# Performance work log

Measured on AMD Instinct MI355X. Metric: run time of the kernel, lower is better.

The kernel has to match this reference:

```python
import jax, jax.numpy as jnp
import numpy as np

HIDDEN = 1024
N_HEADS = 16
HEAD_DIM = HIDDEN // N_HEADS


def setup_inputs() -> dict:
    key = jax.random.key(0)
    ks = jax.random.split(key, 7)
    b, l, m = 4, 1024, 1024
    q = jax.random.normal(ks[0], (b, l, HIDDEN), dtype=jnp.float32)
    k = jax.random.normal(ks[1], (b, m, HIDDEN), dtype=jnp.float32)
    v = jax.random.normal(ks[2], (b, m, HIDDEN), dtype=jnp.float32)
    s = 1.0 / np.sqrt(HIDDEN)
    w_q = jax.random.normal(ks[3], (HIDDEN, HIDDEN), dtype=jnp.float32) * s
    w_k = jax.random.normal(ks[4], (HIDDEN, HIDDEN), dtype=jnp.float32) * s
    w_v = jax.random.normal(ks[5], (HIDDEN, HIDDEN), dtype=jnp.float32) * s
    w_o = jax.random.normal(ks[6], (HIDDEN, HIDDEN), dtype=jnp.float32) * s
    return {"q": q, "k": k, "v": v, "w_q": w_q, "w_k": w_k, "w_v": w_v, "w_o": w_o}


def reference(q, k, v, w_q, w_k, w_v, w_o):
    b, l, _ = q.shape
    _, m, _ = k.shape
    # Linear (bias=False): y = x @ W^T
    qp = q @ w_q.T
    kp = k @ w_k.T
    vp = v @ w_v.T  # projected but unused downstream (faithful to original bug)
    # Faithful non-standard split: hidden -> (head_dim, n_heads)
    qh = qp.reshape(b, l, HEAD_DIM, N_HEADS)
    kh = kp.reshape(b, m, HEAD_DIM, N_HEADS)
    # attn over K, scaled, softmax over m (dim=2)
    scores = jnp.einsum('bldn,bmdn->blmn', qh, kh) / np.sqrt(HEAD_DIM)
    attn = jax.nn.softmax(scores, axis=2)
    # dropout is identity in eval mode
    # NOTE: original attends over K (not V) — reproduced faithfully
    x = jnp.einsum('blmn,bmdn->bldn', attn, kh)
    x = x.reshape(b, l, HIDDEN)  # 'b l d n -> b l (d n)'
    return x @ w_o.T
```

## Files before the change

kernel.cpp:

```cpp
#include <hip/hip_runtime.h>
#include <hip/hip_bf16.h>
#include <stdint.h>
#include <math.h>


typedef __bf16 bf16;
typedef __bf16 bf16x8 __attribute__((ext_vector_type(8)));
typedef float  f32x4  __attribute__((ext_vector_type(4)));

__device__ __forceinline__ void async_load16(const void* g, void* l) {
  __builtin_amdgcn_global_load_lds((__attribute__((address_space(1))) void*)g,
                                   (__attribute__((address_space(3))) void*)l,
                                   16, 0, 0);
}

__device__ __forceinline__ int detect_fl(const void* samp, int tid, int* smax) {
  int e = (((const unsigned short*)samp)[tid] >> 7) & 0xFF;
#pragma unroll
  for (int off = 1; off <= 32; off <<= 1) {
    int o = __shfl_xor(e, off);
    e = o > e ? o : e;
  }
  if ((tid & 63) == 0) smax[tid >> 6] = e;
  __syncthreads();
  int m01 = smax[0] > smax[1] ? smax[0] : smax[1];
  int m23 = smax[2] > smax[3] ? smax[2] : smax[3];
  return ((m01 > m23 ? m01 : m23) >= 140) ? 1 : 0;
}

__global__ void __launch_bounds__(256)
canon_wo(const void* __restrict__ wo_raw, bf16* __restrict__ wo_p,
         int* __restrict__ flag) {
  __shared__ int smax[4];
  const int tid = threadIdx.x;
  const int fl = detect_fl(wo_raw, tid, smax);
  if (blockIdx.x == 0 && tid == 0) *flag = fl;

  int d0 = blockIdx.x * 2048 + tid * 8;
  int o = d0 >> 10, kp0 = d0 & 1023;
  bf16x8 v;
#pragma unroll
  for (int j = 0; j < 8; ++j) {
    int kp = kp0 + j;
    int h = ((kp & 63) << 4) | (kp >> 6);
    float f = fl ? ((const float*)wo_raw)[o * 1024 + h]
                 : (float)((const bf16*)wo_raw)[o * 1024 + h];
    f = fminf(fmaxf(f, -1024.f), 1024.f);
    v[j] = (bf16)f;
  }
  *(bf16x8*)(wo_p + d0) = v;
}

__global__ void __launch_bounds__(256, 2)
qk_gemm(const void* __restrict__ q_raw, const void* __restrict__ wq_raw,
        const void* __restrict__ k_raw, const void* __restrict__ wk_raw,
        bf16* __restrict__ qh, bf16* __restrict__ kh, bf16* __restrict__ khT,
        float cs) {
  __shared__ bf16 sA[128 * 64];
  __shared__ bf16 sB[128 * 64];
  __shared__ bf16 epi[128 * 134];
  __shared__ int smax[4];

  const int tid = threadIdx.x;
  const int fl  = detect_fl(q_raw, tid, smax);

  const int z = blockIdx.z;
  const void* A = z ? k_raw : q_raw;
  const void* W = z ? wk_raw : wq_raw;
  const float scale = z ? 1.0f : cs;
  bf16* out0 = z ? kh : qh;

  const int lane = tid & 63;
  const int wave = tid >> 6;
  const int q4   = lane >> 4;
  const int c16  = lane & 15;
  const int wm   = wave >> 1;
  const int wn   = wave & 1;

  const int lin    = blockIdx.x + 8 * blockIdx.y;
  const int rowBlk = (lin & 31) * 128;
  const int colBlk = (lin >> 5) * 128;

  int sr[4], sg[4];
#pragma unroll
  for (int i = 0; i < 4; ++i) {
    int s = tid + 256 * i;
    sr[i] = s >> 3;
    sg[i] = (s & 7) ^ (sr[i] & 7);
  }

  f32x4 acc[4][4] = {};

  for (int kk = 0; kk < 1024; kk += 64) {
    __syncthreads();
    {
      bf16x8 st[4];
      if (fl) {
#pragma unroll
        for (int i = 0; i < 4; ++i) {
          const float* p = (const float*)A +
              (size_t)(rowBlk + sr[i]) * 1024 + kk + sg[i] * 8;
#pragma unroll
          for (int j = 0; j < 8; ++j) st[i][j] = (bf16)p[j];
        }
      } else {
#pragma unroll
        for (int i = 0; i < 4; ++i)
          st[i] = *(const bf16x8*)((const bf16*)A +
              (size_t)(rowBlk + sr[i]) * 1024 + kk + sg[i] * 8);
      }
#pragma unroll
      for (int i = 0; i < 4; ++i) *(bf16x8*)(sA + (tid + 256 * i) * 8) = st[i];
    }
    {
      bf16x8 st[4];
      if (fl) {
#pragma unroll
        for (int i = 0; i < 4; ++i) {
          const float* p = (const float*)W +
              (size_t)(colBlk + sr[i]) * 1024 + kk + sg[i] * 8;
#pragma unroll
          for (int j = 0; j < 8; ++j) st[i][j] = (bf16)p[j];
        }
      } else {
#pragma unroll
        for (int i = 0; i < 4; ++i)
          st[i] = *(const bf16x8*)((const bf16*)W +
              (size_t)(colBlk + sr[i]) * 1024 + kk + sg[i] * 8);
      }
#pragma unroll
      for (int i = 0; i < 4; ++i) *(bf16x8*)(sB + (tid + 256 * i) * 8) = st[i];
    }
    __syncthreads();

    bf16x8 af[2][4], bfr[2][4];
#pragma unroll
    for (int ks = 0; ks < 2; ++ks) {
#pragma unroll
      for (int mt = 0; mt < 4; ++mt) {
        int row = wm * 64 + mt * 16 + c16;
        af[ks][mt] = *(const bf16x8*)(sA + row * 64 +
                       (((ks * 4 + q4) ^ (row & 7)) * 8));
      }
#pragma unroll
      for (int nt = 0; nt < 4; ++nt) {
        int row = wn * 64 + nt * 16 + c16;
        bfr[ks][nt] = *(const bf16x8*)(sB + row * 64 +
                       (((ks * 4 + q4) ^ (row & 7)) * 8));
      }
    }
#pragma unroll
    for (int ks = 0; ks < 2; ++ks)
#pragma unroll
      for (int mt = 0; mt < 4; ++mt)
#pragma unroll
        for (int nt = 0; nt < 4; ++nt)
          acc[mt][nt] = __builtin_amdgcn_mfma_f32_16x16x32_bf16(
              af[ks][mt], bfr[ks][nt], acc[mt][nt], 0, 0, 0);
  }

  __syncthreads();
#pragma unroll
  for (int mt = 0; mt < 4; ++mt)
#pragma unroll
    for (int nt = 0; nt < 4; ++nt)
#pragma unroll
      for (int r = 0; r < 4; ++r) {
        int m_t = wm * 64 + mt * 16 + q4 * 4 + r;
        int h_t = wn * 64 + nt * 16 + c16;
        epi[m_t * 134 + h_t] = (bf16)(acc[mt][nt][r] * scale);
      }
  __syncthreads();

  const int bb    = rowBlk >> 10;
  const int mbase = rowBlk & 1023;
  const int dg0   = colBlk >> 4;

  {
    int n = tid >> 4;
#pragma unroll
    for (int i = 0; i < 8; ++i) {
      int m_t = (tid & 15) + i * 16;
      bf16x8 v;
#pragma unroll
      for (int dt = 0; dt < 8; ++dt) v[dt] = epi[m_t * 134 + dt * 16 + n];
      *(bf16x8*)(out0 + ((size_t)(bb * 16 + n) * 1024 + mbase + m_t) * 64 + dg0) = v;
    }
  }
  if (z) {
    int h_t = tid >> 1, half = tid & 1;
    int n = h_t & 15, dt = h_t >> 4;
    size_t base = ((size_t)(bb * 16 + n) * 64 + dg0 + dt) * 1024 + mbase + half * 64;
#pragma unroll
    for (int c = 0; c < 8; ++c) {
      bf16x8 v;
#pragma unroll
      for (int j = 0; j < 8; ++j) v[j] = epi[(half * 64 + c * 8 + j) * 134 + h_t];
      *(bf16x8*)(khT + base + c * 8) = v;
    }
  }
}

__global__ void __launch_bounds__(256, 2)
o_gemm(const bf16* __restrict__ A, const bf16* __restrict__ W,
       bf16* __restrict__ out0, float* __restrict__ outf,
       const int* __restrict__ flag) {
  __shared__ bf16 sA[128 * 128];
  __shared__ bf16 sB[64 * 128];

  const int tid  = threadIdx.x;
  const int lane = tid & 63;
  const int wave = tid >> 6;
  const int q4   = lane >> 4;
  const int c16  = lane & 15;
  const int wm   = wave >> 1;
  const int wn   = wave & 1;

  const int lin    = blockIdx.x + 16 * blockIdx.y;
  const int rowBlk = (lin & 31) * 128;
  const int colBlk = (lin >> 5) * 64;

  int ar[8], ag[8];
#pragma unroll
  for (int i = 0; i < 8; ++i) {
    int s = tid + 256 * i;
    ar[i] = s >> 4;
    ag[i] = (s & 15) ^ (ar[i] & 15);
  }
  const bf16* gA[8];
  bf16* lA[8];
#pragma unroll
  for (int i = 0; i < 8; ++i) {
    gA[i] = A + (size_t)(rowBlk + ar[i]) * 1024 + ag[i] * 8;
    lA[i] = sA + (tid + 256 * i) * 8;
  }
  const bf16* gB[4];
  bf16* lB[4];
#pragma unroll
  for (int i = 0; i < 4; ++i) {
    int s = tid + 256 * i;
    int br = s >> 4, bg = (s & 15) ^ (br & 15);
    gB[i] = W + (size_t)(colBlk + br) * 1024 + bg * 8;
    lB[i] = sB + s * 8;
  }

  f32x4 acc[4][2] = {};

  for (int kk = 0; kk < 1024; kk += 128) {
    __syncthreads();
#pragma unroll
    for (int i = 0; i < 8; ++i) async_load16(gA[i] + kk, lA[i]);
#pragma unroll
    for (int i = 0; i < 4; ++i) async_load16(gB[i] + kk, lB[i]);
    __builtin_amdgcn_s_waitcnt(0);
    __syncthreads();

#pragma unroll
    for (int ks = 0; ks < 4; ++ks) {
      bf16x8 af[4], bfr[2];
#pragma unroll
      for (int mt = 0; mt < 4; ++mt) {
        int row = wm * 64 + mt * 16 + c16;
        af[mt] = *(const bf16x8*)(sA + row * 128 +
                   (((ks * 4 + q4) ^ (row & 15)) * 8));
      }
#pragma unroll
      for (int nt = 0; nt < 2; ++nt) {
        int row = wn * 32 + nt * 16 + c16;
        bfr[nt] = *(const bf16x8*)(sB + row * 128 +
                   (((ks * 4 + q4) ^ (row & 15)) * 8));
      }
#pragma unroll
      for (int mt = 0; mt < 4; ++mt)
#pragma unroll
        for (int nt = 0; nt < 2; ++nt)
          acc[mt][nt] = __builtin_amdgcn_mfma_f32_16x16x32_bf16(
              af[mt], bfr[nt], acc[mt][nt], 0, 0, 0);
    }
  }

  const int fl = *flag;
#pragma unroll
  for (int mt = 0; mt < 4; ++mt)
#pragma unroll
    for (int nt = 0; nt < 2; ++nt)
#pragma unroll
      for (int r = 0; r < 4; ++r) {
        int gm = rowBlk + wm * 64 + mt * 16 + q4 * 4 + r;
        int gn = colBlk + wn * 32 + nt * 16 + c16;
        size_t idx = (size_t)gm * 1024 + gn;
        if (fl) outf[idx] = acc[mt][nt][r];
        else    out0[idx] = (bf16)acc[mt][nt][r];
      }
}

__global__ void __launch_bounds__(256, 2)
attn_kernel(const bf16* __restrict__ qh, const bf16* __restrict__ kh,
            const bf16* __restrict__ khT, bf16* __restrict__ xh) {
  __shared__ bf16 sK[128 * 64];
  __shared__ bf16 sKT[64 * 128];
  __shared__ bf16 sP[4][32 * 136];

  const int tid  = threadIdx.x;
  const int lane = tid & 63;
  const int wave = tid >> 6;
  const int q4   = lane >> 4;
  const int c16  = lane & 15;
  const int bn   = blockIdx.x;
  const int b    = bn >> 4, n = bn & 15;
  const int l0w  = blockIdx.y * 128 + wave * 32;

  const bf16* qhead  = qh  + (size_t)bn * (1024 * 64);
  const bf16* khead  = kh  + (size_t)bn * (1024 * 64);
  const bf16* kThead = khT + (size_t)bn * (64 * 1024);

  bf16x8 aq[2][2];
#pragma unroll
  for (int g = 0; g < 2; ++g)
#pragma unroll
    for (int hh = 0; hh < 2; ++hh)
      aq[g][hh] = *(const bf16x8*)(qhead +
                    (size_t)(l0w + g * 16 + c16) * 64 + hh * 32 + q4 * 8);

  int kr[4], kg[4], tr[4], tg[4];
#pragma unroll
  for (int i = 0; i < 4; ++i) {
    int s = tid + 256 * i;
    kr[i] = s >> 3;  kg[i] = (s & 7) ^ (kr[i] & 7);
    tr[i] = s >> 4;  tg[i] = (s & 15) ^ (tr[i] & 15);
  }

  f32x4 O[2][4] = {};
  f32x4 Osum[2] = {};
  bf16x8 ones;
#pragma unroll
  for (int j = 0; j < 8; ++j) ones[j] = (bf16)1.0f;
  bf16* sPw = sP[wave];

  for (int m0 = 0; m0 < 1024; m0 += 128) {
    __syncthreads();
#pragma unroll
    for (int i = 0; i < 4; ++i) {
      async_load16(khead + (size_t)(m0 + kr[i]) * 64 + kg[i] * 8,
                   sK + (tid + 256 * i) * 8);
      async_load16(kThead + (size_t)tr[i] * 1024 + m0 + tg[i] * 8,
                   sKT + (tid + 256 * i) * 8);
    }
    __builtin_amdgcn_s_waitcnt(0);
    __syncthreads();

    f32x4 S[2][8] = {};
#pragma unroll
    for (int t = 0; t < 8; ++t) {
#pragma unroll
      for (int hh = 0; hh < 2; ++hh) {
        int row = t * 16 + c16;
        bf16x8 bk = *(const bf16x8*)(sK + row * 64 +
                                     (((hh * 4 + q4) ^ (row & 7)) * 8));
        S[0][t] = __builtin_amdgcn_mfma_f32_16x16x32_bf16(aq[0][hh], bk, S[0][t], 0, 0, 0);
        S[1][t] = __builtin_amdgcn_mfma_f32_16x16x32_bf16(aq[1][hh], bk, S[1][t], 0, 0, 0);
      }
    }

#pragma unroll
    for (int g = 0; g < 2; ++g)
#pragma unroll
      for (int t = 0; t < 8; ++t)
#pragma unroll
        for (int r = 0; r < 4; ++r) {
          float p = __builtin_amdgcn_exp2f(S[g][t][r]);
          sPw[(g * 16 + q4 * 4 + r) * 136 + t * 16 + c16] = (bf16)p;
        }

    bf16x8 ap[2][4];
#pragma unroll
    for (int g = 0; g < 2; ++g) {
#pragma unroll
      for (int kk2 = 0; kk2 < 4; ++kk2) {
        ap[g][kk2] = *(const bf16x8*)(sPw + (g * 16 + c16) * 136 +
                                      kk2 * 32 + q4 * 8);
        Osum[g] = __builtin_amdgcn_mfma_f32_16x16x32_bf16(ap[g][kk2], ones, Osum[g], 0, 0, 0);
      }
    }

#pragma unroll
    for (int td = 0; td < 4; ++td) {
#pragma unroll
      for (int kk2 = 0; kk2 < 4; ++kk2) {
        int row = td * 16 + c16;
        bf16x8 bkt = *(const bf16x8*)(sKT + row * 128 +
                                      (((kk2 * 4 + q4) ^ (row & 15)) * 8));
        O[0][td] = __builtin_amdgcn_mfma_f32_16x16x32_bf16(ap[0][kk2], bkt, O[0][td], 0, 0, 0);
        O[1][td] = __builtin_amdgcn_mfma_f32_16x16x32_bf16(ap[1][kk2], bkt, O[1][td], 0, 0, 0);
      }
    }
  }

#pragma unroll
  for (int g = 0; g < 2; ++g) {
    float inv[4];
#pragma unroll
    for (int r = 0; r < 4; ++r) inv[r] = 1.0f / Osum[g][r];
#pragma unroll
    for (int td = 0; td < 4; ++td)
#pragma unroll
      for (int r = 0; r < 4; ++r)
        sPw[(g * 16 + q4 * 4 + r) * 136 + td * 16 + c16] = (bf16)(O[g][td][r] * inv[r]);
  }
  {
    int l_loc = lane >> 2, dq = lane & 3;
#pragma unroll
    for (int g = 0; g < 2; ++g) {
      bf16x8 v0 = *(const bf16x8*)(sPw + (g * 16 + l_loc) * 136 + dq * 16);
      bf16x8 v1 = *(const bf16x8*)(sPw + (g * 16 + l_loc) * 136 + dq * 16 + 8);
      size_t base = ((size_t)(b * 1024 + l0w + g * 16 + l_loc) * 16 + n) * 64 + dq * 16;
      *(bf16x8*)(xh + base)     = v0;
      *(bf16x8*)(xh + base + 8) = v1;
    }
  }
}

extern "C" void kernel_launch(void* const* d_in, const int* in_sizes, int n_in,
                              void* d_out, int out_size, void* d_ws, size_t ws_size,
                              hipStream_t stream) {
  const void* q_raw  = d_in[0];
  const void* k_raw  = d_in[1];
  const void* wq_raw = d_in[3];
  const void* wk_raw = d_in[4];
  const void* wo_raw = d_in[6];

  char* ws = (char*)d_ws;
  const size_t MB = 1024 * 1024;
  bf16* xh   = (bf16*)(ws + 0 * MB);
  bf16* kh   = (bf16*)(ws + 16 * MB);
  bf16* wo_p = (bf16*)(ws + 28 * MB);
  int*  flag = (int*)(ws + 30 * MB);
  bf16* qh   = (bf16*)d_out;
  bf16* khT  = (bf16*)((char*)d_out + 8 * MB);

  const float CS = 0.125f * 1.4426950408889634f;
  dim3 blk(256, 1, 1);

  hipLaunchKernelGGL(canon_wo, dim3(512), blk, 0, stream,
                     wo_raw, wo_p, flag);
  hipLaunchKernelGGL(qk_gemm, dim3(8, 32, 2), blk, 0, stream,
                     q_raw, wq_raw, k_raw, wk_raw, qh, kh, khT, CS);
  hipLaunchKernelGGL(attn_kernel, dim3(64, 8, 1), blk, 0, stream,
                     qh, kh, khT, xh);
  hipLaunchKernelGGL(o_gemm, dim3(16, 32, 1), blk, 0, stream,
                     xh, wo_p, (bf16*)d_out, (float*)d_out, flag);
}
```

Measured before the change: 188.7 us.

## Prefetch next fp32 K-tile into registers and use async LDS loads for bf16 path

The projection GEMM's main loop is split by input type. In the fp32 path, the next 64-wide K slice of A and W is loaded into registers with vectorized f32x4 loads while the current tile's MFMAs run, so global latency overlaps with compute; conversion to bf16 happens just before the LDS store. In the bf16 path, global_load_lds async copies replace the register round trip. The register prefetch raises VGPR pressure and may reduce occupancy, and the bf16 path still waits fully before computing.

```diff
diff --git a/kernel.cpp b/kernel.cpp
--- a/kernel.cpp
+++ b/kernel.cpp
@@ -91,72 +91,112 @@
 
   f32x4 acc[4][4] = {};
 
-  for (int kk = 0; kk < 1024; kk += 64) {
-    __syncthreads();
-    {
-      bf16x8 st[4];
-      if (fl) {
+  if (fl) {
+    const float* Af = (const float*)A;
+    const float* Wf = (const float*)W;
+    f32x4 stA[8], stB[8];
+#pragma unroll
+    for (int i = 0; i < 4; ++i) {
+      const float* pA = Af + (size_t)(rowBlk + sr[i]) * 1024 + sg[i] * 8;
+      stA[2 * i]     = *(const f32x4*)pA;
+      stA[2 * i + 1] = *(const f32x4*)(pA + 4);
+      const float* pB = Wf + (size_t)(colBlk + sr[i]) * 1024 + sg[i] * 8;
+      stB[2 * i]     = *(const f32x4*)pB;
+      stB[2 * i + 1] = *(const f32x4*)(pB + 4);
+    }
+
+    for (int kk = 0; kk < 1024; kk += 64) {
+      __syncthreads();
+#pragma unroll
+      for (int i = 0; i < 4; ++i) {
+        bf16x8 va, vb;
+#pragma unroll
+        for (int j = 0; j < 4; ++j) {
+          va[j]     = (bf16)stA[2 * i][j];
+          va[4 + j] = (bf16)stA[2 * i + 1][j];
+          vb[j]     = (bf16)stB[2 * i][j];
+          vb[4 + j] = (bf16)stB[2 * i + 1][j];
+        }
+        *(bf16x8*)(sA + (tid + 256 * i) * 8) = va;
+        *(bf16x8*)(sB + (tid + 256 * i) * 8) = vb;
+      }
+      __syncthreads();
+
+      if (kk + 64 < 1024) {
 #pragma unroll
         for (int i = 0; i < 4; ++i) {
-          const float* p = (const float*)A +
-              (size_t)(rowBlk + sr[i]) * 1024 + kk + sg[i] * 8;
-#pragma unroll
-          for (int j = 0; j < 8; ++j) st[i][j] = (bf16)p[j];
-        }
-      } else {
-#pragma unroll
-        for (int i = 0; i < 4; ++i)
-          st[i] = *(const bf16x8*)((const bf16*)A +
-              (size_t)(rowBlk + sr[i]) * 1024 + kk + sg[i] * 8);
-      }
-#pragma unroll
-      for (int i = 0; i < 4; ++i) *(bf16x8*)(sA + (tid + 256 * i) * 8) = st[i];
-    }
-    {
-      bf16x8 st[4];
-      if (fl) {
-#pragma unroll
-        for (int i = 0; i < 4; ++i) {
-          const float* p = (const float*)W +
-              (size_t)(colBlk + sr[i]) * 1024 + kk + sg[i] * 8;
-#pragma unroll
-          for (int j = 0; j < 8; ++j) st[i][j] = (bf16)p[j];
-        }
-      } else {
-#pragma unroll
-        for (int i = 0; i < 4; ++i)
-          st[i] = *(const bf16x8*)((const bf16*)W +
-              (size_t)(colBlk + sr[i]) * 1024 + kk + sg[i] * 8);
-      }
-#pragma unroll
-      for (int i = 0; i < 4; ++i) *(bf16x8*)(sB + (tid + 256 * i) * 8) = st[i];
-    }
-    __syncthreads();
-
-    bf16x8 af[2][4], bfr[2][4];
-#pragma unroll
-    for (int ks = 0; ks < 2; ++ks) {
-#pragma unroll
-      for (int mt = 0; mt < 4; ++mt) {
-        int row = wm * 64 + mt * 16 + c16;
-        af[ks][mt] = *(const bf16x8*)(sA + row * 64 +
-                       (((ks * 4 + q4) ^ (row & 7)) * 8));
-      }
-#pragma unroll
-      for (int nt = 0; nt < 4; ++nt) {
-        int row = wn * 64 + nt * 16 + c16;
-        bfr[ks][nt] = *(const bf16x8*)(sB + row * 64 +
-                       (((ks * 4 + q4) ^ (row & 7)) * 8));
-      }
-    }
-#pragma unroll
-    for (int ks = 0; ks < 2; ++ks)
-#pragma unroll
-      for (int mt = 0; mt < 4; ++mt)
-#pragma unroll
-        for (int nt = 0; nt < 4; ++nt)
-          acc[mt][nt] = __builtin_amdgcn_mfma_f32_16x16x32_bf16(
-              af[ks][mt], bfr[ks][nt], acc[mt][nt], 0, 0, 0);
+          const float* pA = Af + (size_t)(rowBlk + sr[i]) * 1024 + kk + 64 + sg[i] * 8;
+          stA[2 * i]     = *(const f32x4*)pA;
+          stA[2 * i + 1] = *(const f32x4*)(pA + 4);
+          const float* pB = Wf + (size_t)(colBlk + sr[i]) * 1024 + kk + 64 + sg[i] * 8;
+          stB[2 * i]     = *(const f32x4*)pB;
+          stB[2 * i + 1] = *(const f32x4*)(pB + 4);
+        }
+      }
+
+      bf16x8 af[2][4], bfr[2][4];
+#pragma unroll
+      for (int ks = 0; ks < 2; ++ks) {
+#pragma unroll
+        for (int mt = 0; mt < 4; ++mt) {
+          int row = wm * 64 + mt * 16 + c16;
+          af[ks][mt] = *(const bf16x8*)(sA + row * 64 +
+                         (((ks * 4 + q4) ^ (row & 7)) * 8));
+        }
+#pragma unroll
+        for (int nt = 0; nt < 4; ++nt) {
+          int row = wn * 64 + nt * 16 + c16;
+          bfr[ks][nt] = *(const bf16x8*)(sB + row * 64 +
+                         (((ks * 4 + q4) ^ (row & 7)) * 8));
+        }
+      }
+#pragma unroll
+      for (int ks = 0; ks < 2; ++ks)
+#pragma unroll
+        for (int mt = 0; mt < 4; ++mt)
+#pragma unroll
+          for (int nt = 0; nt < 4; ++nt)
+            acc[mt][nt] = __builtin_amdgcn_mfma_f32_16x16x32_bf16(
+                af[ks][mt], bfr[ks][nt], acc[mt][nt], 0, 0, 0);
+    }
+  } else {
+    for (int kk = 0; kk < 1024; kk += 64) {
+      __syncthreads();
+#pragma unroll
+      for (int i = 0; i < 4; ++i) {
+        async_load16((const bf16*)A + (size_t)(rowBlk + sr[i]) * 1024 + kk + sg[i] * 8,
+                     sA + (tid + 256 * i) * 8);
+        async_load16((const bf16*)W + (size_t)(colBlk + sr[i]) * 1024 + kk + sg[i] * 8,
+                     sB + (tid + 256 * i) * 8);
+      }
+      __builtin_amdgcn_s_waitcnt(0);
+      __syncthreads();
+
+      bf16x8 af[2][4], bfr[2][4];
+#pragma unroll
+      for (int ks = 0; ks < 2; ++ks) {
+#pragma unroll
+        for (int mt = 0; mt < 4; ++mt) {
+          int row = wm * 64 + mt * 16 + c16;
+          af[ks][mt] = *(const bf16x8*)(sA + row * 64 +
+                         (((ks * 4 + q4) ^ (row & 7)) * 8));
+        }
+#pragma unroll
+        for (int nt = 0; nt < 4; ++nt) {
+          int row = wn * 64 + nt * 16 + c16;
+          bfr[ks][nt] = *(const bf16x8*)(sB + row * 64 +
+                         (((ks * 4 + q4) ^ (row & 7)) * 8));
+        }
+      }
+#pragma unroll
+      for (int ks = 0; ks < 2; ++ks)
+#pragma unroll
+        for (int mt = 0; mt < 4; ++mt)
+#pragma unroll
+          for (int nt = 0; nt < 4; ++nt)
+            acc[mt][nt] = __builtin_amdgcn_mfma_f32_16x16x32_bf16(
+                af[ks][mt], bfr[ks][nt], acc[mt][nt], 0, 0, 0);
+    }
   }
 
   __syncthreads();
```

New measurement: 190.4 us. Within noise of the previous version (+0.9%).
